# Kernel tuning notes

Hardware: AMD Instinct MI355X
Metric: run time of the kernel (lower is better)

The kernel has to match this reference:

```python
import jax, jax.numpy as jnp
import numpy as np

B, S, E, F, R, T = 2, 2048, 768, 3072, 4, 128
H = 12  # num_heads
HD = E // H
HID = 128  # lora_mlp_dim


def _lin(key, out_f, in_f):
    bound = 1.0 / np.sqrt(in_f)
    return jax.random.uniform(key, (out_f, in_f), jnp.float32, -bound, bound)


def _bias(key, out_f, in_f):
    bound = 1.0 / np.sqrt(in_f)
    return jax.random.uniform(key, (out_f,), jnp.float32, -bound, bound)


def setup_inputs() -> dict:
    key = jax.random.key(0)
    ks = jax.random.split(key, 20)
    return {
        "src": jax.random.normal(ks[0], (B, S, E), jnp.float32),
        "task_embedding": jax.random.normal(ks[1], (B, S, T), jnp.float32),
        "norm1_w": jnp.ones((E,), jnp.float32),
        "norm2_w": jnp.ones((E,), jnp.float32),
        "in_proj_w": _lin(ks[2], 3 * E, E),      # MHA qkv, bias=False
        "out_proj_w": _lin(ks[3], E, E),          # MHA out, bias=False
        "ffn1_w": _lin(ks[4], F, E), "ffn1_b": _bias(ks[5], F, E),
        "ffn2_w": _lin(ks[6], E, F), "ffn2_b": _bias(ks[7], E, F),
        "hA_w1": _lin(ks[8], HID, T), "hA_b1": _bias(ks[9], HID, T),
        "hA_w2": _lin(ks[10], F * R, HID), "hA_b2": _bias(ks[11], F * R, HID),
        "hB_w1": _lin(ks[12], HID, T), "hB_b1": _bias(ks[13], HID, T),
        "hB_w2": _lin(ks[14], R * E, HID), "hB_b2": _bias(ks[15], R * E, HID),
    }


def _rmsnorm(x, w):
    eps = jnp.finfo(x.dtype).eps
    return x * jax.lax.rsqrt(jnp.mean(x * x, axis=-1, keepdims=True) + eps) * w


def reference(src, task_embedding, norm1_w, norm2_w, in_proj_w, out_proj_w,
              ffn1_w, ffn1_b, ffn2_w, ffn2_b,
              hA_w1, hA_b1, hA_w2, hA_b2, hB_w1, hB_b1, hB_w2, hB_b2):
    # --- self-attention block (pre-RMSNorm) ---
    x = _rmsnorm(src, norm1_w)
    qkv = jnp.einsum('bse,fe->bsf', x, in_proj_w)  # [B,S,3E]
    q, k, v = jnp.split(qkv, 3, axis=-1)
    q = q.reshape(B, S, H, HD).transpose(0, 2, 1, 3)
    k = k.reshape(B, S, H, HD).transpose(0, 2, 1, 3)
    v = v.reshape(B, S, H, HD).transpose(0, 2, 1, 3)
    scores = jnp.einsum('bhqd,bhkd->bhqk', q, k) / jnp.sqrt(jnp.float32(HD))
    attn = jax.nn.softmax(scores, axis=-1)
    ctx = jnp.einsum('bhqk,bhkd->bhqd', attn, v)
    ctx = ctx.transpose(0, 2, 1, 3).reshape(B, S, E)
    attn_out = jnp.einsum('bse,fe->bsf', ctx, out_proj_w)
    src = src + attn_out

    # --- FFN block with per-token hypernetwork LoRA on linear1 ---
    x = _rmsnorm(src, norm2_w)
    # hypernetwork: MLP(task) -> per-token A [F,R], B [R,E]
    hA = jax.nn.relu(jnp.einsum('bst,ht->bsh', task_embedding, hA_w1) + hA_b1)
    A_params = (jnp.einsum('bsh,fh->bsf', hA, hA_w2) + hA_b2).reshape(B, S, F, R)
    hB = jax.nn.relu(jnp.einsum('bst,ht->bsh', task_embedding, hB_w1) + hB_b1)
    B_params = (jnp.einsum('bsh,fh->bsf', hB, hB_w2) + hB_b2).reshape(B, S, R, E)

    base = jnp.einsum('bse,fe->bsf', x, ffn1_w) + ffn1_b  # [B,S,F]
    inter = jnp.einsum('bse,bsre->bsr', x, B_params)       # [B,S,R]
    adapt = jnp.einsum('bsr,bsfr->bsf', inter, A_params)   # [B,S,F]
    h = jax.nn.relu(base + adapt)
    out2 = jnp.einsum('bsf,ef->bse', h, ffn2_w) + ffn2_b
    return src + out2
```

## Files before the change

### kernel.cpp

```cpp
#include <hip/hip_runtime.h>
#include <math.h>

#define NB 2
#define NS 2048
#define NE 768
#define NF 3072
#define NHEAD 12
#define NTOK 4096
#define LDW 1344
#define VTS 2176

typedef __bf16 bf16;
typedef __bf16 bf16x2 __attribute__((ext_vector_type(2)));
typedef __bf16 bf16x4 __attribute__((ext_vector_type(4)));
typedef __bf16 bf16x8 __attribute__((ext_vector_type(8)));
typedef float  f32x4  __attribute__((ext_vector_type(4)));

__device__ __forceinline__ f32x4 mfma_bf16(bf16x8 a, bf16x8 b, f32x4 c) {
  return __builtin_amdgcn_mfma_f32_16x16x32_bf16(a, b, c, 0, 0, 0);
}

__device__ __forceinline__ float fast_exp2(float x) {
#if __has_builtin(__builtin_amdgcn_exp2f)
  return __builtin_amdgcn_exp2f(x);
#else
  return exp2f(x);
#endif
}

__device__ __forceinline__ void glds16(const void* g, void* l) {
  __builtin_amdgcn_global_load_lds((const __attribute__((address_space(1))) void*)g,
                                   (__attribute__((address_space(3))) void*)l,
                                   16, 0, 0);
}

__device__ __forceinline__ void pipe_barrier_keep4() {
  asm volatile("s_waitcnt vmcnt(4)" ::: "memory");
  __builtin_amdgcn_s_barrier();
  __builtin_amdgcn_sched_barrier(0);
}
__device__ __forceinline__ void pipe_barrier_drain() {
  asm volatile("s_waitcnt vmcnt(0)" ::: "memory");
  __builtin_amdgcn_s_barrier();
  __builtin_amdgcn_sched_barrier(0);
}

__device__ __forceinline__ void swz_xy(int& bx, int& by) {
  int gx = gridDim.x;
  int i = by*gx + bx;
  int xcd = i & 7, s = i >> 3;
  int bands = gridDim.y >> 3;
  by = xcd*bands + s / gx;
  bx = s % gx;
}

__global__ void prep_kernel(const float* __restrict__ in_proj, const float* __restrict__ out_proj,
                            const float* __restrict__ ffn1_w, const float* __restrict__ ffn1_b,
                            const float* __restrict__ ffn2_w,
                            const float* __restrict__ hA_w1, const float* __restrict__ hA_b1,
                            const float* __restrict__ hA_w2, const float* __restrict__ hA_b2,
                            const float* __restrict__ hB_w1, const float* __restrict__ hB_b1,
                            const float* __restrict__ hB_w2,
                            const float* __restrict__ task,
                            bf16* __restrict__ Wqkv, bf16* __restrict__ Wo, bf16* __restrict__ W2,
                            bf16* __restrict__ W1ab, float* __restrict__ b1ab,
                            bf16* __restrict__ WBp, bf16* __restrict__ Wc,
                            bf16* __restrict__ task_bf)
{
  __shared__ float tb[64*130];
  int stride = gridDim.x * blockDim.x;
  int t0 = blockIdx.x * blockDim.x + threadIdx.x;
  const float QS = 0.125f * 1.44269504088896f;
  for (int i = t0; i < (2304*768)/4; i += stride) {
    float4 v = ((const float4*)in_proj)[i];
    float sc = (i < (768*768)/4) ? QS : 1.0f;
    *(bf16x4*)(Wqkv + i*4) = (bf16x4){(bf16)(v.x*sc), (bf16)(v.y*sc), (bf16)(v.z*sc), (bf16)(v.w*sc)};
  }
  for (int i = t0; i < (768*768)/4; i += stride) {
    float4 v = ((const float4*)out_proj)[i];
    *(bf16x4*)(Wo + i*4) = (bf16x4){(bf16)v.x, (bf16)v.y, (bf16)v.z, (bf16)v.w};
  }
  for (int i = t0; i < (768*3072)/4; i += stride) {
    float4 v = ((const float4*)ffn2_w)[i];
    *(bf16x4*)(W2 + i*4) = (bf16x4){(bf16)v.x, (bf16)v.y, (bf16)v.z, (bf16)v.w};
  }
  for (int i = t0; i < (NTOK*128)/4; i += stride) {
    float4 v = ((const float4*)task)[i];
    *(bf16x4*)(task_bf + i*4) = (bf16x4){(bf16)v.x, (bf16)v.y, (bf16)v.z, (bf16)v.w};
  }
  for (int i = t0; i < 256*128;  i += stride)
    W1ab[i] = (bf16)(i < 128*128 ? hA_w1[i] : hB_w1[i - 128*128]);
  for (int i = t0; i < 256; i += stride) b1ab[i] = (i < 128) ? hA_b1[i] : hB_b1[i-128];

  for (int j0 = blockIdx.x*64; j0 < 3072; j0 += gridDim.x*64) {
    __syncthreads();
    for (int i = threadIdx.x; i < 64*128; i += 256) {
      int jr = i >> 7, hh = i & 127;
      tb[jr*130 + hh] = hB_w2[(long)(j0 + jr)*128 + hh];
    }
    __syncthreads();
    int r = j0 / 768, e0 = j0 % 768;
    for (int i = threadIdx.x; i < 128*64; i += 256) {
      int hh = i >> 6, jr = i & 63;
      WBp[(long)(r*128 + hh)*768 + e0 + jr] = (bf16)tb[jr*130 + hh];
    }
  }

  for (int f = blockIdx.x; f < 3072; f += gridDim.x) {
    const float* hrow = hA_w2 + (long)f*512;
    bf16* wrow = Wc + (long)f*LDW;
    for (int c = threadIdx.x; c < 768; c += 256) wrow[c] = (bf16)ffn1_w[(long)f*768 + c];
    for (int i = threadIdx.x; i < 512; i += 256) {
      int r = i >> 7, h = i & 127;
      wrow[768 + h*4 + r] = (bf16)hrow[i];
    }
    if (threadIdx.x < 4)        wrow[1280 + threadIdx.x] = (bf16)hA_b2[f*4 + threadIdx.x];
    else if (threadIdx.x == 4)  wrow[1284] = (bf16)ffn1_b[f];
    else if (threadIdx.x < 64)  wrow[1280 + threadIdx.x] = (bf16)0.f;
  }
}

__global__ __launch_bounds__(256) void rmsnorm_k(const float* __restrict__ x,
                                                 const float* __restrict__ w,
                                                 bf16* __restrict__ out, int ld_out)
{
  __shared__ float red[4];
  long t = blockIdx.x;
  const float* xr = x + t*NE;
  float ss = 0.f;
  #pragma unroll
  for (int i = 0; i < 3; i++) { float v = xr[threadIdx.x + i*256]; ss += v*v; }
  #pragma unroll
  for (int d = 1; d < 64; d <<= 1) ss += __shfl_xor(ss, d, 64);
  if ((threadIdx.x & 63) == 0) red[threadIdx.x >> 6] = ss;
  __syncthreads();
  float tot = red[0] + red[1] + red[2] + red[3];
  float scale = rsqrtf(tot * (1.f/768.f) + 1.1920928955078125e-07f);
  #pragma unroll
  for (int i = 0; i < 3; i++) {
    int idx = threadIdx.x + i*256;
    out[t*ld_out + idx] = (bf16)(xr[idx] * scale * w[idx]);
  }
}

template<typename OutT, bool RELU, bool BIAS, bool RES>
__global__ __launch_bounds__(256) void gemm_bt_sw(const bf16* __restrict__ A,
                                                  const bf16* __restrict__ Bm,
                                                  OutT* __restrict__ C,
                                                  const float* __restrict__ bias,
                                                  const float* __restrict__ res,
                                                  int K, int lda, int ldb, int ldc)
{
  __shared__ bf16 As[3][128*32];
  __shared__ bf16 Bs[3][128*32];
  const int tid = threadIdx.x;
  int bx = blockIdx.x, by = blockIdx.y;
  swz_xy(bx, by);
  const int m0 = by * 128;
  const int n0 = bx * 128;
  const int w = tid >> 6, lane = tid & 63;
  const int quad = lane >> 4, l16 = lane & 15;
  const int wy = w >> 1, wx = w & 1;

  f32x4 acc[4][4];
  #pragma unroll
  for (int i = 0; i < 4; i++)
    #pragma unroll
    for (int j = 0; j < 4; j++) acc[i][j] = (f32x4){0.f,0.f,0.f,0.f};

  const int i0 = tid, i1 = tid + 256;
  const int R0 = i0 >> 3, cc0 = (i0 & 7) ^ (R0 & 7), r0 = 2*R0 + (cc0 >> 2), ch0 = (cc0 & 3) * 8;
  const int R1 = i1 >> 3, cc1 = (i1 & 7) ^ (R1 & 7), r1 = 2*R1 + (cc1 >> 2), ch1 = (cc1 & 3) * 8;
  const bf16* pA0 = A  + (long)(m0 + r0)*lda + ch0;
  const bf16* pA1 = A  + (long)(m0 + r1)*lda + ch1;
  const bf16* pB0 = Bm + (long)(n0 + r0)*ldb + ch0;
  const bf16* pB1 = Bm + (long)(n0 + r1)*ldb + ch1;
  auto stage = [&](int buf) {
    glds16(pA0, (void*)(&As[buf][i0*8]));
    glds16(pA1, (void*)(&As[buf][i1*8]));
    glds16(pB0, (void*)(&Bs[buf][i0*8]));
    glds16(pB1, (void*)(&Bs[buf][i1*8]));
    pA0 += 32; pA1 += 32; pB0 += 32; pB1 += 32;
  };

  stage(0);
  stage(1);
  pipe_barrier_keep4();

  const int Rh = l16 >> 1;
  const int ppq = ((l16 & 1) << 2) | quad;
  const int jfr = ppq ^ Rh;
  const int nsteps = K >> 5;
  int cur = 0, nx2 = 2;
  for (int s = 0; s < nsteps; ++s) {
    const bool more = (s + 2 < nsteps);
    if (more) stage(nx2);

    bf16x8 af[4], bfr[4];
    #pragma unroll
    for (int mi = 0; mi < 4; ++mi)
      af[mi] = *(const bf16x8*)(&As[cur][(wy*32 + mi*8 + Rh)*64 + jfr*8]);
    #pragma unroll
    for (int ni = 0; ni < 4; ++ni)
      bfr[ni] = *(const bf16x8*)(&Bs[cur][(wx*32 + ni*8 + Rh)*64 + jfr*8]);
    #pragma unroll
    for (int mi = 0; mi < 4; ++mi)
      #pragma unroll
      for (int ni = 0; ni < 4; ++ni)
        acc[mi][ni] = mfma_bf16(af[mi], bfr[ni], acc[mi][ni]);

    if (more) pipe_barrier_keep4();
    else      pipe_barrier_drain();
    cur = (cur == 2) ? 0 : cur + 1;
    nx2 = (nx2 == 2) ? 0 : nx2 + 1;
  }

  #pragma unroll
  for (int mi = 0; mi < 4; ++mi)
    #pragma unroll
    for (int ni = 0; ni < 4; ++ni) {
      int col = n0 + wx*64 + ni*16 + l16;
      #pragma unroll
      for (int r = 0; r < 4; ++r) {
        long row = m0 + wy*64 + mi*16 + quad*4 + r;
        float v = acc[mi][ni][r];
        if (BIAS) v += bias[col];
        if (RES)  v += res[row*ldc + col];
        if (RELU) v = v > 0.f ? v : 0.f;
        C[row*ldc + col] = (OutT)v;
      }
    }
}

template<typename OutT, bool RELU, bool BIAS, bool RES>
__global__ __launch_bounds__(256) void gemm64(const bf16* __restrict__ A,
                                              const bf16* __restrict__ Bm,
                                              OutT* __restrict__ C,
                                              const float* __restrict__ bias,
                                              const float* __restrict__ res,
                                              int K, int lda, int ldb, int ldc)
{
  __shared__ bf16 As[3][64*64];
  __shared__ bf16 Bs[3][64*64];
  const int tid = threadIdx.x;
  int bx = blockIdx.x, by = blockIdx.y;
  swz_xy(bx, by);
  const int m0 = by * 64, n0 = bx * 64;
  const int w = tid >> 6, lane = tid & 63;
  const int quad = lane >> 4, l16 = lane & 15;
  const int wy = w >> 1, wx = w & 1;
  const int sw = l16 & 7;

  f32x4 acc[2][2];
  #pragma unroll
  for (int i = 0; i < 2; i++)
    #pragma unroll
    for (int j = 0; j < 2; j++) acc[i][j] = (f32x4){0.f,0.f,0.f,0.f};

  const int c0 = tid, c1 = tid + 256;
  const int r0 = c0 >> 3, g0 = ((c0 & 7) ^ (r0 & 7)) * 8;
  const int r1 = c1 >> 3, g1 = ((c1 & 7) ^ (r1 & 7)) * 8;
  const bf16* pA0 = A  + (long)(m0 + r0)*lda + g0;
  const bf16* pA1 = A  + (long)(m0 + r1)*lda + g1;
  const bf16* pB0 = Bm + (long)(n0 + r0)*ldb + g0;
  const bf16* pB1 = Bm + (long)(n0 + r1)*ldb + g1;
  auto stage = [&](int buf) {
    glds16(pA0, (void*)(&As[buf][c0*8]));
    glds16(pA1, (void*)(&As[buf][c1*8]));
    glds16(pB0, (void*)(&Bs[buf][c0*8]));
    glds16(pB1, (void*)(&Bs[buf][c1*8]));
    pA0 += 64; pA1 += 64; pB0 += 64; pB1 += 64;
  };

  const int nsteps = K >> 6;
  stage(0);
  if (nsteps > 1) stage(1);
  pipe_barrier_keep4();

  int cur = 0, nx2 = 2;
  for (int s = 0; s < nsteps; ++s) {
    const bool more = (s + 2 < nsteps);
    if (more) stage(nx2);

    bf16x8 af[2][2], bfr[2][2];
    #pragma unroll
    for (int mi = 0; mi < 2; ++mi)
      #pragma unroll
      for (int kb = 0; kb < 2; ++kb)
        af[mi][kb] = *(const bf16x8*)(&As[cur][(wy*32 + mi*16 + l16)*64 + (((kb*4 + quad) ^ sw))*8]);
    #pragma unroll
    for (int ni = 0; ni < 2; ++ni)
      #pragma unroll
      for (int kb = 0; kb < 2; ++kb)
        bfr[ni][kb] = *(const bf16x8*)(&Bs[cur][(wx*32 + ni*16 + l16)*64 + (((kb*4 + quad) ^ sw))*8]);
    #pragma unroll
    for (int kb = 0; kb < 2; ++kb)
      #pragma unroll
      for (int mi = 0; mi < 2; ++mi)
        #pragma unroll
        for (int ni = 0; ni < 2; ++ni)
          acc[mi][ni] = mfma_bf16(af[mi][kb], bfr[ni][kb], acc[mi][ni]);

    if (more) pipe_barrier_keep4();
    else      pipe_barrier_drain();
    cur = (cur == 2) ? 0 : cur + 1;
    nx2 = (nx2 == 2) ? 0 : nx2 + 1;
  }

  #pragma unroll
  for (int mi = 0; mi < 2; ++mi)
    #pragma unroll
    for (int ni = 0; ni < 2; ++ni) {
      int col = n0 + wx*32 + ni*16 + l16;
      #pragma unroll
      for (int r = 0; r < 4; ++r) {
        long row = m0 + wy*32 + mi*16 + quad*4 + r;
        float v = acc[mi][ni][r];
        if (BIAS) v += bias[col];
        if (RES)  v += res[row*ldc + col];
        if (RELU) v = v > 0.f ? v : 0.f;
        C[row*ldc + col] = (OutT)v;
      }
    }
}

__global__ __launch_bounds__(256) void gemm_qkv64(const bf16* __restrict__ A,
                                                  const bf16* __restrict__ Bm,
                                                  bf16* __restrict__ Qkv,
                                                  bf16* __restrict__ Vt)
{
  __shared__ bf16 As[3][64*64];
  __shared__ bf16 Bs[3][64*64];
  const int tid = threadIdx.x;
  int bx = blockIdx.x, by = blockIdx.y;
  swz_xy(bx, by);
  const int m0 = by * 64, n0 = bx * 64;
  const int w = tid >> 6, lane = tid & 63;
  const int quad = lane >> 4, l16 = lane & 15;
  const int wy = w >> 1, wx = w & 1;
  const int sw = l16 & 7;

  f32x4 acc[2][2];
  #pragma unroll
  for (int i = 0; i < 2; i++)
    #pragma unroll
    for (int j = 0; j < 2; j++) acc[i][j] = (f32x4){0.f,0.f,0.f,0.f};

  const int c0 = tid, c1 = tid + 256;
  const int r0 = c0 >> 3, g0 = ((c0 & 7) ^ (r0 & 7)) * 8;
  const int r1 = c1 >> 3, g1 = ((c1 & 7) ^ (r1 & 7)) * 8;
  const bf16* pA0 = A  + (long)(m0 + r0)*768 + g0;
  const bf16* pA1 = A  + (long)(m0 + r1)*768 + g1;
  const bf16* pB0 = Bm + (long)(n0 + r0)*768 + g0;
  const bf16* pB1 = Bm + (long)(n0 + r1)*768 + g1;
  auto stage = [&](int buf) {
    glds16(pA0, (void*)(&As[buf][c0*8]));
    glds16(pA1, (void*)(&As[buf][c1*8]));
    glds16(pB0, (void*)(&Bs[buf][c0*8]));
    glds16(pB1, (void*)(&Bs[buf][c1*8]));
    pA0 += 64; pA1 += 64; pB0 += 64; pB1 += 64;
  };

  stage(0);
  stage(1);
  pipe_barrier_keep4();

  int cur = 0, nx2 = 2;
  for (int s = 0; s < 12; ++s) {
    const bool more = (s + 2 < 12);
    if (more) stage(nx2);

    bf16x8 af[2][2], bfr[2][2];
    #pragma unroll
    for (int mi = 0; mi < 2; ++mi)
      #pragma unroll
      for (int kb = 0; kb < 2; ++kb)
        af[mi][kb] = *(const bf16x8*)(&As[cur][(wy*32 + mi*16 + l16)*64 + (((kb*4 + quad) ^ sw))*8]);
    #pragma unroll
    for (int ni = 0; ni < 2; ++ni)
      #pragma unroll
      for (int kb = 0; kb < 2; ++kb)
        bfr[ni][kb] = *(const bf16x8*)(&Bs[cur][(wx*32 + ni*16 + l16)*64 + (((kb*4 + quad) ^ sw))*8]);
    #pragma unroll
    for (int kb = 0; kb < 2; ++kb)
      #pragma unroll
      for (int mi = 0; mi < 2; ++mi)
        #pragma unroll
        for (int ni = 0; ni < 2; ++ni)
          acc[mi][ni] = mfma_bf16(af[mi][kb], bfr[ni][kb], acc[mi][ni]);

    if (more) pipe_barrier_keep4();
    else      pipe_barrier_drain();
    cur = (cur == 2) ? 0 : cur + 1;
    nx2 = (nx2 == 2) ? 0 : nx2 + 1;
  }

  const int bb = m0 >> 11;
  #pragma unroll
  for (int mi = 0; mi < 2; ++mi)
    #pragma unroll
    for (int ni = 0; ni < 2; ++ni) {
      int col = n0 + wx*32 + ni*16 + l16;
      #pragma unroll
      for (int r = 0; r < 4; ++r) {
        long row = m0 + wy*32 + mi*16 + quad*4 + r;
        bf16 v = (bf16)acc[mi][ni][r];
        if (col < 1536) {
          Qkv[row*2304 + col] = v;
        } else {
          int vc = col - 1536;
          int hh = vc >> 6, d = vc & 63;
          long srow = row & (NS-1);
          Vt[((long)(bb*NHEAD + hh)*64 + d)*VTS + srow] = v;
        }
      }
    }
}

__global__ __launch_bounds__(256, 2) void flash_attn(const bf16* __restrict__ Qkv,
                                                     const bf16* __restrict__ Vt,
                                                     bf16* __restrict__ Ctx)
{
  __shared__ bf16 Ks[2][2][64*64];
  __shared__ bf16 Vs[2][2][64*64];

  const int tid = threadIdx.x;
  const int w = tid >> 6, lane = tid & 63;
  const int quad = lane >> 4, l16 = lane & 15;
  const int pair = w >> 1, qw = w & 1;
  int bx = blockIdx.x, by = blockIdx.y;
  swz_xy(bx, by);
  const int bh = by;
  const int b = bh / NHEAD, h = bh % NHEAD;
  const int q0 = bx * 64;

  bf16x8 qf[2][2];
  #pragma unroll
  for (int mi = 0; mi < 2; ++mi) {
    const long tq = (long)(b*NS + q0 + qw*32 + mi*16 + l16);
    qf[mi][0] = *(const bf16x8*)(Qkv + tq*2304 + h*64 + quad*8);
    qf[mi][1] = *(const bf16x8*)(Qkv + tq*2304 + h*64 + 32 + quad*8);
  }

  bf16x8 ones;
  #pragma unroll
  for (int j = 0; j < 8; ++j) ones[j] = (bf16)1.0f;

  f32x4 o[2][4];
  f32x4 o5[2];
  #pragma unroll
  for (int mi = 0; mi < 2; ++mi) {
    o5[mi] = (f32x4){0.f,0.f,0.f,0.f};
    #pragma unroll
    for (int i = 0; i < 4; i++) o[mi][i] = (f32x4){0.f,0.f,0.f,0.f};
  }

  const int ptid = tid & 127;
  const bf16* kp[4];
  const bf16* vp[4];
  int cc[4];
  #pragma unroll
  for (int i = 0; i < 4; ++i) {
    int c = ptid + i*128;
    cc[i] = c;
    int r = c >> 3, g = ((c & 7) ^ (r & 7)) * 8;
    kp[i] = Qkv + (long)(b*NS + pair*1024 + r)*2304 + 768 + h*64 + g;
    vp[i] = Vt + ((long)bh*64 + r)*VTS + pair*1024 + g;
  }
  auto stage = [&](int buf) {
    #pragma unroll
    for (int i = 0; i < 4; ++i) {
      glds16(kp[i], (void*)(&Ks[pair][buf][cc[i]*8]));
      glds16(vp[i], (void*)(&Vs[pair][buf][cc[i]*8]));
      kp[i] += (long)64*2304; vp[i] += 64;
    }
  };

  auto body = [&](int cur) {
    bf16x8 kfr[4][2];
    #pragma unroll
    for (int nt = 0; nt < 4; ++nt)
      #pragma unroll
      for (int kb = 0; kb < 2; ++kb)
        kfr[nt][kb] = *(const bf16x8*)(&Ks[pair][cur][(nt*16 + l16)*64 + (((kb*4 + quad) ^ (l16 & 7)))*8]);

    bf16x8 pf[2][2];
    #pragma unroll
    for (int mi = 0; mi < 2; ++mi) {
      f32x4 s[4];
      #pragma unroll
      for (int nt = 0; nt < 4; ++nt) {
        s[nt] = (f32x4){0.f,0.f,0.f,0.f};
        #pragma unroll
        for (int kb = 0; kb < 2; ++kb)
          s[nt] = mfma_bf16(kfr[nt][kb], qf[mi][kb], s[nt]);
      }
      #pragma unroll
      for (int nt = 0; nt < 4; ++nt)
        #pragma unroll
        for (int r = 0; r < 4; ++r)
          pf[mi][nt >> 1][(nt & 1)*4 + r] = (bf16)fast_exp2(s[nt][r]);
    }
    #pragma unroll
    for (int ntp = 0; ntp < 2; ++ntp) {
      bf16x8 vf[4];
      #pragma unroll
      for (int dt = 0; dt < 4; ++dt) {
        int row = dt*16 + l16;
        int cA = ntp*4 + (quad >> 1);
        int base = row*64 + (quad & 1)*4;
        bf16x4 va = *(const bf16x4*)(&Vs[pair][cur][base + ((cA       ^ (row & 7)) << 3)]);
        bf16x4 vb = *(const bf16x4*)(&Vs[pair][cur][base + (((cA + 2) ^ (row & 7)) << 3)]);
        vf[dt] = (bf16x8){va[0],va[1],va[2],va[3], vb[0],vb[1],vb[2],vb[3]};
      }
      #pragma unroll
      for (int mi = 0; mi < 2; ++mi) {
        #pragma unroll
        for (int dt = 0; dt < 4; ++dt)
          o[mi][dt] = mfma_bf16(pf[mi][ntp], vf[dt], o[mi][dt]);
        o5[mi] = mfma_bf16(pf[mi][ntp], ones, o5[mi]);
      }
    }
  };

  stage(0);
  __builtin_amdgcn_s_waitcnt(0);
  __syncthreads();

  for (int t = 0; t < 16; t += 2) {
    stage(1);
    body(0);
    __builtin_amdgcn_s_waitcnt(0);
    __syncthreads();
    if (t + 2 < 16) stage(0);
    body(1);
    __builtin_amdgcn_s_waitcnt(0);
    __syncthreads();
  }

  float* Of = (float*)&Ks[0][0][0];
  float* Lf = Of + 64*68;
  const int rbase = qw*32;
  if (pair == 1) {
    #pragma unroll
    for (int mi = 0; mi < 2; ++mi)
      #pragma unroll
      for (int r = 0; r < 4; ++r) {
        int row = rbase + mi*16 + quad*4 + r;
        if (l16 == 0) Lf[row] = o5[mi][r];
        #pragma unroll
        for (int dt = 0; dt < 4; ++dt)
          Of[row*68 + dt*16 + l16] = o[mi][dt][r];
      }
  }
  __syncthreads();
  if (pair == 0) {
    #pragma unroll
    for (int mi = 0; mi < 2; ++mi)
      #pragma unroll
      for (int r = 0; r < 4; ++r) {
        int row = rbase + mi*16 + quad*4 + r;
        float inv = 1.f / (o5[mi][r] + Lf[row]);
        long trow = (long)(b*NS + q0 + row);
        #pragma unroll
        for (int dt = 0; dt < 4; ++dt)
          Ctx[trow*NE + h*64 + dt*16 + l16] =
            (bf16)((o[mi][dt][r] + Of[row*68 + dt*16 + l16]) * inv);
      }
  }
}

__global__ __launch_bounds__(256) void build_g(const bf16* __restrict__ HAB,
                                               const float* __restrict__ P,
                                               const float* __restrict__ hB_b2,
                                               bf16* __restrict__ Aext)
{
  long t = blockIdx.x*4 + (threadIdx.x >> 6);
  int lane = threadIdx.x & 63;
  const bf16* xr = Aext + t*LDW;
  float acc[4] = {0.f, 0.f, 0.f, 0.f};
  #pragma unroll
  for (int k = 0; k < 6; ++k) {
    int idx = lane + k*64;
    bf16x2 xv = *(const bf16x2*)(xr + idx*2);
    float x0 = (float)xv[0], x1 = (float)xv[1];
    #pragma unroll
    for (int r = 0; r < 4; ++r)
      acc[r] += x0 * hB_b2[r*768 + idx*2] + x1 * hB_b2[r*768 + idx*2 + 1];
  }
  const bf16* hB = HAB + t*256 + 128;
  const float* Pr = P + t*512;
  #pragma unroll
  for (int k = 0; k < 2; ++k) {
    int h = lane + k*64;
    float hv = (float)hB[h];
    #pragma unroll
    for (int r = 0; r < 4; ++r) acc[r] += hv * Pr[r*128 + h];
  }
  #pragma unroll
  for (int r = 0; r < 4; ++r)
    #pragma unroll
    for (int d = 1; d < 64; d <<= 1) acc[r] += __shfl_xor(acc[r], d, 64);

  bf16* grow = Aext + t*LDW + 768;
  const bf16* hA = HAB + t*256;
  bf16x8 gv;
  #pragma unroll
  for (int j = 0; j < 8; ++j) {
    int idx = lane*8 + j;
    int h = idx >> 2, r = idx & 3;
    gv[j] = (bf16)((float)hA[h] * acc[r]);
  }
  *(bf16x8*)(grow + lane*8) = gv;
  if (lane < 4)       Aext[t*LDW + 1280 + lane] = (bf16)acc[lane];
  else if (lane == 4) Aext[t*LDW + 1284] = (bf16)1.0f;
  else                Aext[t*LDW + 1280 + lane] = (bf16)0.f;
}

extern "C" void kernel_launch(void* const* d_in, const int* in_sizes, int n_in,
                              void* d_out, int out_size, void* d_ws, size_t ws_size,
                              hipStream_t stream)
{
  const float* src      = (const float*)d_in[0];
  const float* task     = (const float*)d_in[1];
  const float* norm1_w  = (const float*)d_in[2];
  const float* norm2_w  = (const float*)d_in[3];
  const float* in_proj  = (const float*)d_in[4];
  const float* out_proj = (const float*)d_in[5];
  const float* ffn1_w   = (const float*)d_in[6];
  const float* ffn1_b   = (const float*)d_in[7];
  const float* ffn2_w   = (const float*)d_in[8];
  const float* ffn2_b   = (const float*)d_in[9];
  const float* hA_w1    = (const float*)d_in[10];
  const float* hA_b1    = (const float*)d_in[11];
  const float* hA_w2    = (const float*)d_in[12];
  const float* hA_b2    = (const float*)d_in[13];
  const float* hB_w1    = (const float*)d_in[14];
  const float* hB_b1    = (const float*)d_in[15];
  const float* hB_w2    = (const float*)d_in[16];
  const float* hB_b2    = (const float*)d_in[17];
  float* out = (float*)d_out;

  char* ws = (char*)d_ws;
  size_t off = 0;
  auto alloc = [&](size_t bytes) { size_t o = off; off += (bytes + 255) & ~(size_t)255; return o; };
  bf16*  Wqkv   = (bf16*)(ws + alloc(2304*768*2));
  bf16*  Wo     = (bf16*)(ws + alloc(768*768*2));
  bf16*  W2     = (bf16*)(ws + alloc(768*3072*2));
  bf16*  W1ab   = (bf16*)(ws + alloc(256*128*2));
  float* b1ab   = (float*)(ws + alloc(256*4));
  bf16*  WBp    = (bf16*)(ws + alloc(512*768*2));
  bf16*  Wc     = (bf16*)(ws + alloc((size_t)3072*LDW*2));
  bf16*  taskbf = (bf16*)(ws + alloc((size_t)NTOK*128*2));
  bf16*  XC     = (bf16*)(ws + alloc((size_t)NTOK*768*2));
  char*  QKVH   = ws + alloc(25559040);
  bf16*  Qkv    = (bf16*)QKVH;
  bf16*  Vt     = (bf16*)(QKVH + 18874368);
  bf16*  Hbuf   = (bf16*)QKVH;
  float* Src2   = (float*)(ws + alloc((size_t)NTOK*768*4));
  bf16*  Aext   = (bf16*)(ws + alloc((size_t)NTOK*LDW*2));
  bf16*  HAB    = (bf16*)(ws + alloc((size_t)NTOK*256*2));
  float* P      = (float*)(ws + alloc((size_t)NTOK*512*4));

  prep_kernel<<<dim3(1280), 256, 0, stream>>>(in_proj, out_proj, ffn1_w, ffn1_b, ffn2_w,
      hA_w1, hA_b1, hA_w2, hA_b2, hB_w1, hB_b1, hB_w2, task,
      Wqkv, Wo, W2, W1ab, b1ab, WBp, Wc, taskbf);
  rmsnorm_k<<<dim3(NTOK), 256, 0, stream>>>(src, norm1_w, XC, 768);
  gemm_qkv64<<<dim3(36,64), 256, 0, stream>>>(XC, Wqkv, Qkv, Vt);
  flash_attn<<<dim3(32,24), 256, 0, stream>>>(Qkv, Vt, XC);
  gemm64<float,false,false,true><<<dim3(12,64), 256, 0, stream>>>(XC, Wo, Src2, nullptr, src, 768, 768, 768, 768);
  rmsnorm_k<<<dim3(NTOK), 256, 0, stream>>>(Src2, norm2_w, Aext, LDW);
  gemm64<bf16,true,true,false><<<dim3(4,64), 256, 0, stream>>>(taskbf, W1ab, HAB, b1ab, nullptr, 128, 128, 128, 256);
  gemm64<float,false,false,false><<<dim3(8,64), 256, 0, stream>>>(Aext, WBp, P, nullptr, nullptr, 768, LDW, 768, 512);
  build_g<<<dim3(NTOK/4), 256, 0, stream>>>(HAB, P, hB_b2, Aext);
  gemm_bt_sw<bf16,true,false,false><<<dim3(24,32), 256, 0, stream>>>(Aext, Wc, Hbuf, nullptr, nullptr, 1312, LDW, LDW, 3072);
  gemm64<float,false,true,true><<<dim3(12,64), 256, 0, stream>>>(Hbuf, W2, out, ffn2_b, Src2, 3072, 3072, 3072, 768);
}
```

Baseline: 209.7 us.

## Add 256x256-tile 512-thread GEMM for the LoRA-augmented FFN1 projection

Adds a new bf16 GEMM kernel with 256x256 output tiles, 512 threads and a double-buffered LDS pipeline split into two K halves. It interleaves async global-to-LDS loads with MFMA phases under explicit barriers and priority hints. It replaces the 128x128 tiled kernel for the FFN1 plus adapter GEMM, aiming for more data reuse per tile and fewer LDS loads per MFMA. With only 192 blocks the grid leaves some CUs idle. K is now rounded up to the full padded width of 1344, which assumes the pad columns hold zeros.

Result: no change. 211.0 us (+0.6%).

```diff
diff --git a/kernel.cpp b/kernel.cpp
--- a/kernel.cpp
+++ b/kernel.cpp
@@ -141,6 +141,140 @@
     int idx = threadIdx.x + i*256;
     out[t*ld_out + idx] = (bf16)(xr[idx] * scale * w[idx]);
   }
+}
+
+__global__ __launch_bounds__(512, 2) void gemm256(const bf16* __restrict__ A,
+                                                  const bf16* __restrict__ Bm,
+                                                  bf16* __restrict__ C,
+                                                  int nt, int lda, int ldb, int ldc)
+{
+  __shared__ bf16 As[2][2][256*32];
+  __shared__ bf16 Bs[2][2][256*32];
+  const int tid = threadIdx.x;
+  int bx = blockIdx.x, by = blockIdx.y;
+  swz_xy(bx, by);
+  const int m0 = by * 256, n0 = bx * 256;
+  const int w = tid >> 6, lane = tid & 63;
+  const int quad = lane >> 4, l16 = lane & 15;
+  const int wm = w >> 2, wn = w & 3;
+
+  f32x4 acc[8][4];
+  #pragma unroll
+  for (int i = 0; i < 8; i++)
+    #pragma unroll
+    for (int j = 0; j < 4; j++) acc[i][j] = (f32x4){0.f,0.f,0.f,0.f};
+
+  const int R0 = tid >> 3, cc0 = (tid & 7) ^ (R0 & 7);
+  const int r0 = 2*R0 + (cc0 >> 2), ch0 = (cc0 & 3)*8;
+  const bf16* pa = A  + (long)(m0 + r0)*lda + ch0;
+  const bf16* pb = Bm + (long)(n0 + r0)*ldb + ch0;
+  const long paStep = (long)128*lda, pbStep = (long)128*ldb;
+
+  auto stageA = [&](int buf, int kh, int kt) {
+    const bf16* s = pa + kt + kh*32;
+    glds16(s,          (void*)(&As[buf][kh][tid*8]));
+    glds16(s + paStep, (void*)(&As[buf][kh][(tid + 512)*8]));
+  };
+  auto stageB = [&](int buf, int kh, int kt) {
+    const bf16* s = pb + kt + kh*32;
+    glds16(s,          (void*)(&Bs[buf][kh][tid*8]));
+    glds16(s + pbStep, (void*)(&Bs[buf][kh][(tid + 512)*8]));
+  };
+
+  const int Rh = l16 >> 1;
+  const int jfr = (((l16 & 1) << 2) | quad) ^ Rh;
+  const int aBase = wm*64, bBase = wn*32;
+
+  auto barrier = [] { __builtin_amdgcn_s_barrier(); __builtin_amdgcn_sched_barrier(0); };
+
+  stageA(0, 0, 0); stageB(0, 0, 0); stageA(0, 1, 0); stageB(0, 1, 0);
+  asm volatile("s_waitcnt vmcnt(4)" ::: "memory");
+  barrier();
+
+  for (int t = 0; t < nt; ++t) {
+    const int cur = t & 1, nb = cur ^ 1;
+    const bool more = (t + 1 < nt);
+    const int kt1 = (t + 1) << 6;
+    bf16x8 af[4], bfr[4];
+
+    #pragma unroll
+    for (int j = 0; j < 4; ++j)
+      af[j] = *(const bf16x8*)(&As[cur][0][(aBase + j*8 + Rh)*64 + jfr*8]);
+    #pragma unroll
+    for (int ni = 0; ni < 4; ++ni)
+      bfr[ni] = *(const bf16x8*)(&Bs[cur][0][(bBase + ni*8 + Rh)*64 + jfr*8]);
+    if (more) stageA(nb, 0, kt1);
+    barrier();
+    __builtin_amdgcn_s_setprio(1);
+    #pragma unroll
+    for (int j = 0; j < 4; ++j)
+      #pragma unroll
+      for (int ni = 0; ni < 4; ++ni)
+        acc[j][ni] = mfma_bf16(af[j], bfr[ni], acc[j][ni]);
+    __builtin_amdgcn_s_setprio(0);
+    barrier();
+
+    #pragma unroll
+    for (int j = 0; j < 4; ++j)
+      af[j] = *(const bf16x8*)(&As[cur][0][(aBase + 32 + j*8 + Rh)*64 + jfr*8]);
+    if (more) stageB(nb, 0, kt1);
+    barrier();
+    __builtin_amdgcn_s_setprio(1);
+    #pragma unroll
+    for (int j = 0; j < 4; ++j)
+      #pragma unroll
+      for (int ni = 0; ni < 4; ++ni)
+        acc[4 + j][ni] = mfma_bf16(af[j], bfr[ni], acc[4 + j][ni]);
+    __builtin_amdgcn_s_setprio(0);
+    if (more) asm volatile("s_waitcnt vmcnt(4)" ::: "memory");
+    else      asm volatile("s_waitcnt vmcnt(0)" ::: "memory");
+    barrier();
+
+    #pragma unroll
+    for (int j = 0; j < 4; ++j)
+      af[j] = *(const bf16x8*)(&As[cur][1][(aBase + j*8 + Rh)*64 + jfr*8]);
+    #pragma unroll
+    for (int ni = 0; ni < 4; ++ni)
+      bfr[ni] = *(const bf16x8*)(&Bs[cur][1][(bBase + ni*8 + Rh)*64 + jfr*8]);
+    if (more) stageA(nb, 1, kt1);
+    barrier();
+    __builtin_amdgcn_s_setprio(1);
+    #pragma unroll
+    for (int j = 0; j < 4; ++j)
+      #pragma unroll
+      for (int ni = 0; ni < 4; ++ni)
+        acc[j][ni] = mfma_bf16(af[j], bfr[ni], acc[j][ni]);
+    __builtin_amdgcn_s_setprio(0);
+    barrier();
+
+    #pragma unroll
+    for (int j = 0; j < 4; ++j)
+      af[j] = *(const bf16x8*)(&As[cur][1][(aBase + 32 + j*8 + Rh)*64 + jfr*8]);
+    if (more) stageB(nb, 1, kt1);
+    barrier();
+    __builtin_amdgcn_s_setprio(1);
+    #pragma unroll
+    for (int j = 0; j < 4; ++j)
+      #pragma unroll
+      for (int ni = 0; ni < 4; ++ni)
+        acc[4 + j][ni] = mfma_bf16(af[j], bfr[ni], acc[4 + j][ni]);
+    __builtin_amdgcn_s_setprio(0);
+    if (more) asm volatile("s_waitcnt vmcnt(4)" ::: "memory");
+    barrier();
+  }
+
+  #pragma unroll
+  for (int mi = 0; mi < 8; ++mi)
+    #pragma unroll
+    for (int ni = 0; ni < 4; ++ni) {
+      int col = n0 + wn*64 + ni*16 + l16;
+      #pragma unroll
+      for (int r = 0; r < 4; ++r) {
+        long row = m0 + wm*128 + mi*16 + quad*4 + r;
+        float v = acc[mi][ni][r];
+        C[row*ldc + col] = (bf16)(v > 0.f ? v : 0.f);
+      }
+    }
 }
 
 template<typename OutT, bool RELU, bool BIAS, bool RES>
@@ -673,6 +807,6 @@
   gemm64<bf16,true,true,false><<<dim3(4,64), 256, 0, stream>>>(taskbf, W1ab, HAB, b1ab, nullptr, 128, 128, 128, 256);
   gemm64<float,false,false,false><<<dim3(8,64), 256, 0, stream>>>(Aext, WBp, P, nullptr, nullptr, 768, LDW, 768, 512);
   build_g<<<dim3(NTOK/4), 256, 0, stream>>>(HAB, P, hB_b2, Aext);
-  gemm_bt_sw<bf16,true,false,false><<<dim3(24,32), 256, 0, stream>>>(Aext, Wc, Hbuf, nullptr, nullptr, 1312, LDW, LDW, 3072);
+  gemm256<<<dim3(12,16), 512, 0, stream>>>(Aext, Wc, Hbuf, 21, LDW, LDW, 3072);
   gemm64<float,false,true,true><<<dim3(12,64), 256, 0, stream>>>(Hbuf, W2, out, ffn2_b, Src2, 3072, 3072, 3072, 768);
 }
```

## Rewrite FFN1 GEMM with 128x192 tiles and phased double-buffered MFMA pipeline

Applied to the files above, without the earlier changes.

Replaces the 128x128 triple-buffered FFN1 GEMM with a specialised kernel using 128x192 tiles and 64-wide K steps split into two halves. Loads of the next tile are interleaved with four MFMA phases separated by barriers, with s_setprio raised around the MFMA bursts. The goal is better operand reuse and more overlap of global-to-LDS copies with matrix work. The kernel now processes 1344 K elements (the padded width) rather than 1312, so it relies on the padding columns being zero, and the wider tile launches fewer blocks.

Result: faster. 205.1 us (-2.2%).

```diff
diff --git a/kernel.cpp b/kernel.cpp
--- a/kernel.cpp
+++ b/kernel.cpp
@@ -143,91 +143,143 @@
   }
 }
 
-template<typename OutT, bool RELU, bool BIAS, bool RES>
-__global__ __launch_bounds__(256) void gemm_bt_sw(const bf16* __restrict__ A,
+__global__ __launch_bounds__(256, 2) void gemm_ph(const bf16* __restrict__ A,
                                                   const bf16* __restrict__ Bm,
-                                                  OutT* __restrict__ C,
-                                                  const float* __restrict__ bias,
-                                                  const float* __restrict__ res,
-                                                  int K, int lda, int ldb, int ldc)
+                                                  bf16* __restrict__ C,
+                                                  int nt, int lda, int ldb, int ldc)
 {
-  __shared__ bf16 As[3][128*32];
-  __shared__ bf16 Bs[3][128*32];
+  __shared__ bf16 As[2][2][128*32];
+  __shared__ bf16 Bs[2][2][192*32];
   const int tid = threadIdx.x;
   int bx = blockIdx.x, by = blockIdx.y;
   swz_xy(bx, by);
-  const int m0 = by * 128;
-  const int n0 = bx * 128;
+  const int m0 = by * 128, n0 = bx * 192;
   const int w = tid >> 6, lane = tid & 63;
   const int quad = lane >> 4, l16 = lane & 15;
-  const int wy = w >> 1, wx = w & 1;
-
-  f32x4 acc[4][4];
+  const int wm = w >> 1, wn = w & 1;
+
+  f32x4 acc[4][6];
   #pragma unroll
   for (int i = 0; i < 4; i++)
     #pragma unroll
-    for (int j = 0; j < 4; j++) acc[i][j] = (f32x4){0.f,0.f,0.f,0.f};
-
-  const int i0 = tid, i1 = tid + 256;
-  const int R0 = i0 >> 3, cc0 = (i0 & 7) ^ (R0 & 7), r0 = 2*R0 + (cc0 >> 2), ch0 = (cc0 & 3) * 8;
-  const int R1 = i1 >> 3, cc1 = (i1 & 7) ^ (R1 & 7), r1 = 2*R1 + (cc1 >> 2), ch1 = (cc1 & 3) * 8;
-  const bf16* pA0 = A  + (long)(m0 + r0)*lda + ch0;
-  const bf16* pA1 = A  + (long)(m0 + r1)*lda + ch1;
-  const bf16* pB0 = Bm + (long)(n0 + r0)*ldb + ch0;
-  const bf16* pB1 = Bm + (long)(n0 + r1)*ldb + ch1;
-  auto stage = [&](int buf) {
-    glds16(pA0, (void*)(&As[buf][i0*8]));
-    glds16(pA1, (void*)(&As[buf][i1*8]));
-    glds16(pB0, (void*)(&Bs[buf][i0*8]));
-    glds16(pB1, (void*)(&Bs[buf][i1*8]));
-    pA0 += 32; pA1 += 32; pB0 += 32; pB1 += 32;
+    for (int j = 0; j < 6; j++) acc[i][j] = (f32x4){0.f,0.f,0.f,0.f};
+
+  const int iA0 = tid,      RA0 = iA0 >> 3, cA0 = (iA0 & 7) ^ (RA0 & 7);
+  const int iA1 = tid + 256,RA1 = iA1 >> 3, cA1 = (iA1 & 7) ^ (RA1 & 7);
+  const int iB2 = tid + 512,RB2 = iB2 >> 3, cB2 = (iB2 & 7) ^ (RB2 & 7);
+  const int rA0 = 2*RA0 + (cA0 >> 2), hA0c = (cA0 & 3)*8;
+  const int rA1 = 2*RA1 + (cA1 >> 2), hA1c = (cA1 & 3)*8;
+  const int rB2 = 2*RB2 + (cB2 >> 2), hB2c = (cB2 & 3)*8;
+  const bf16* paA0 = A  + (long)(m0 + rA0)*lda + hA0c;
+  const bf16* paA1 = A  + (long)(m0 + rA1)*lda + hA1c;
+  const bf16* pbB0 = Bm + (long)(n0 + rA0)*ldb + hA0c;
+  const bf16* pbB1 = Bm + (long)(n0 + rA1)*ldb + hA1c;
+  const bf16* pbB2 = Bm + (long)(n0 + rB2)*ldb + hB2c;
+
+  auto stageA = [&](int buf, int kh, int kt) {
+    const int s = kt + kh*32;
+    glds16(paA0 + s, (void*)(&As[buf][kh][tid*8]));
+    glds16(paA1 + s, (void*)(&As[buf][kh][(tid + 256)*8]));
   };
-
-  stage(0);
-  stage(1);
-  pipe_barrier_keep4();
+  auto stageB = [&](int buf, int kh, int kt) {
+    const int s = kt + kh*32;
+    glds16(pbB0 + s, (void*)(&Bs[buf][kh][tid*8]));
+    glds16(pbB1 + s, (void*)(&Bs[buf][kh][(tid + 256)*8]));
+    glds16(pbB2 + s, (void*)(&Bs[buf][kh][(tid + 512)*8]));
+  };
 
   const int Rh = l16 >> 1;
-  const int ppq = ((l16 & 1) << 2) | quad;
-  const int jfr = ppq ^ Rh;
-  const int nsteps = K >> 5;
-  int cur = 0, nx2 = 2;
-  for (int s = 0; s < nsteps; ++s) {
-    const bool more = (s + 2 < nsteps);
-    if (more) stage(nx2);
-
-    bf16x8 af[4], bfr[4];
-    #pragma unroll
-    for (int mi = 0; mi < 4; ++mi)
-      af[mi] = *(const bf16x8*)(&As[cur][(wy*32 + mi*8 + Rh)*64 + jfr*8]);
-    #pragma unroll
-    for (int ni = 0; ni < 4; ++ni)
-      bfr[ni] = *(const bf16x8*)(&Bs[cur][(wx*32 + ni*8 + Rh)*64 + jfr*8]);
-    #pragma unroll
-    for (int mi = 0; mi < 4; ++mi)
-      #pragma unroll
-      for (int ni = 0; ni < 4; ++ni)
-        acc[mi][ni] = mfma_bf16(af[mi], bfr[ni], acc[mi][ni]);
-
-    if (more) pipe_barrier_keep4();
-    else      pipe_barrier_drain();
-    cur = (cur == 2) ? 0 : cur + 1;
-    nx2 = (nx2 == 2) ? 0 : nx2 + 1;
+  const int jfr = (((l16 & 1) << 2) | quad) ^ Rh;
+  const int aBase = wm*32, bBase = wn*48;
+
+  auto barrier = [] { __builtin_amdgcn_s_barrier(); __builtin_amdgcn_sched_barrier(0); };
+
+  stageA(0, 0, 0); stageB(0, 0, 0); stageA(0, 1, 0); stageB(0, 1, 0);
+  asm volatile("s_waitcnt vmcnt(5)" ::: "memory");
+  barrier();
+
+  for (int t = 0; t < nt; ++t) {
+    const int cur = t & 1, nb = cur ^ 1;
+    const bool more = (t + 1 < nt);
+    const int kt1 = (t + 1) << 6;
+    bf16x8 af[2], bfr[6];
+
+    #pragma unroll
+    for (int j = 0; j < 2; ++j)
+      af[j] = *(const bf16x8*)(&As[cur][0][(aBase + j*8 + Rh)*64 + jfr*8]);
+    #pragma unroll
+    for (int ni = 0; ni < 6; ++ni)
+      bfr[ni] = *(const bf16x8*)(&Bs[cur][0][(bBase + ni*8 + Rh)*64 + jfr*8]);
+    if (more) stageA(nb, 0, kt1);
+    barrier();
+    __builtin_amdgcn_s_setprio(1);
+    #pragma unroll
+    for (int j = 0; j < 2; ++j)
+      #pragma unroll
+      for (int ni = 0; ni < 6; ++ni)
+        acc[j][ni] = mfma_bf16(af[j], bfr[ni], acc[j][ni]);
+    __builtin_amdgcn_s_setprio(0);
+    barrier();
+
+    #pragma unroll
+    for (int j = 0; j < 2; ++j)
+      af[j] = *(const bf16x8*)(&As[cur][0][(aBase + 16 + j*8 + Rh)*64 + jfr*8]);
+    if (more) stageB(nb, 0, kt1);
+    barrier();
+    __builtin_amdgcn_s_setprio(1);
+    #pragma unroll
+    for (int j = 0; j < 2; ++j)
+      #pragma unroll
+      for (int ni = 0; ni < 6; ++ni)
+        acc[2 + j][ni] = mfma_bf16(af[j], bfr[ni], acc[2 + j][ni]);
+    __builtin_amdgcn_s_setprio(0);
+    if (more) asm volatile("s_waitcnt vmcnt(5)" ::: "memory");
+    else      asm volatile("s_waitcnt vmcnt(0)" ::: "memory");
+    barrier();
+
+    #pragma unroll
+    for (int j = 0; j < 2; ++j)
+      af[j] = *(const bf16x8*)(&As[cur][1][(aBase + j*8 + Rh)*64 + jfr*8]);
+    #pragma unroll
+    for (int ni = 0; ni < 6; ++ni)
+      bfr[ni] = *(const bf16x8*)(&Bs[cur][1][(bBase + ni*8 + Rh)*64 + jfr*8]);
+    if (more) stageA(nb, 1, kt1);
+    barrier();
+    __builtin_amdgcn_s_setprio(1);
+    #pragma unroll
+    for (int j = 0; j < 2; ++j)
+      #pragma unroll
+      for (int ni = 0; ni < 6; ++ni)
+        acc[j][ni] = mfma_bf16(af[j], bfr[ni], acc[j][ni]);
+    __builtin_amdgcn_s_setprio(0);
+    barrier();
+
+    #pragma unroll
+    for (int j = 0; j < 2; ++j)
+      af[j] = *(const bf16x8*)(&As[cur][1][(aBase + 16 + j*8 + Rh)*64 + jfr*8]);
+    if (more) stageB(nb, 1, kt1);
+    barrier();
+    __builtin_amdgcn_s_setprio(1);
+    #pragma unroll
+    for (int j = 0; j < 2; ++j)
+      #pragma unroll
+      for (int ni = 0; ni < 6; ++ni)
+        acc[2 + j][ni] = mfma_bf16(af[j], bfr[ni], acc[2 + j][ni]);
+    __builtin_amdgcn_s_setprio(0);
+    if (more) asm volatile("s_waitcnt vmcnt(5)" ::: "memory");
+    barrier();
   }
 
   #pragma unroll
   for (int mi = 0; mi < 4; ++mi)
     #pragma unroll
-    for (int ni = 0; ni < 4; ++ni) {
-      int col = n0 + wx*64 + ni*16 + l16;
+    for (int ni = 0; ni < 6; ++ni) {
+      int col = n0 + wn*96 + ni*16 + l16;
       #pragma unroll
       for (int r = 0; r < 4; ++r) {
-        long row = m0 + wy*64 + mi*16 + quad*4 + r;
+        long row = m0 + wm*64 + mi*16 + quad*4 + r;
         float v = acc[mi][ni][r];
-        if (BIAS) v += bias[col];
-        if (RES)  v += res[row*ldc + col];
-        if (RELU) v = v > 0.f ? v : 0.f;
-        C[row*ldc + col] = (OutT)v;
+        C[row*ldc + col] = (bf16)(v > 0.f ? v : 0.f);
       }
     }
 }
@@ -673,6 +725,6 @@
   gemm64<bf16,true,true,false><<<dim3(4,64), 256, 0, stream>>>(taskbf, W1ab, HAB, b1ab, nullptr, 128, 128, 128, 256);
   gemm64<float,false,false,false><<<dim3(8,64), 256, 0, stream>>>(Aext, WBp, P, nullptr, nullptr, 768, LDW, 768, 512);
   build_g<<<dim3(NTOK/4), 256, 0, stream>>>(HAB, P, hB_b2, Aext);
-  gemm_bt_sw<bf16,true,false,false><<<dim3(24,32), 256, 0, stream>>>(Aext, Wc, Hbuf, nullptr, nullptr, 1312, LDW, LDW, 3072);
+  gemm_ph<<<dim3(16,32), 256, 0, stream>>>(Aext, Wc, Hbuf, 21, LDW, LDW, 3072);
   gemm64<float,false,true,true><<<dim3(12,64), 256, 0, stream>>>(Hbuf, W2, out, ffn2_b, Src2, 3072, 3072, 3072, 768);
 }
```
